# Kernel tuning notes

Measured on AMD Instinct MI355X. Metric: run time of the kernel, lower is better.

Reference implementation:

```python
import jax, jax.numpy as jnp
import numpy as np

N, L, HH, WW, E, NH = 8, 300, 96, 96, 256, 8


def setup_inputs() -> dict:
    key = jax.random.key(0)
    ks = jax.random.split(key, 9)
    return {
        "query_row": jax.random.normal(ks[0], (N, L, E), dtype=jnp.float32),
        "query_col": jax.random.normal(ks[1], (N, L, E), dtype=jnp.float32),
        "key_row": jax.random.normal(ks[2], (N, HH, WW, E), dtype=jnp.float32),
        "key_col": jax.random.normal(ks[3], (N, HH, WW, E), dtype=jnp.float32),
        "value": jax.random.normal(ks[4], (N, HH, WW, E), dtype=jnp.float32),
        "in_proj_weight": jax.random.normal(ks[5], (5 * E, E), dtype=jnp.float32) * 0.02,
        "in_proj_bias": jax.random.normal(ks[6], (5 * E,), dtype=jnp.float32) * 0.02,
        "out_proj_weight": jax.random.normal(ks[7], (E, E), dtype=jnp.float32) * 0.02,
        "out_proj_bias": jax.random.normal(ks[8], (E,), dtype=jnp.float32) * 0.02,
        "num_heads": NH,
    }


def reference(query_row, query_col, key_row, key_col, value,
              in_proj_weight, in_proj_bias, out_proj_weight, out_proj_bias,
              num_heads):
    bsz, tgt_len, embed_dim = query_row.shape
    head_dim = embed_dim // num_heads
    scaling = float(head_dim) ** -0.5

    def proj(x, i):
        w = in_proj_weight[i * embed_dim:(i + 1) * embed_dim]
        b = in_proj_bias[i * embed_dim:(i + 1) * embed_dim]
        return x @ w.T + b

    q_row = proj(query_row, 0) * scaling          # (N, L, E)
    q_col = proj(query_col, 1) * scaling          # (N, L, E)
    k_row = proj(key_row, 2).mean(axis=1)         # mean over H -> (N, W, E)
    k_col = proj(key_col, 3).mean(axis=2)         # mean over W -> (N, H, E)
    v = proj(value, 4)                            # (N, H, W, E)

    heads = lambda t: t.reshape(*t.shape[:-1], num_heads, head_dim)
    qr, qc, kr, kc = heads(q_row), heads(q_col), heads(k_row), heads(k_col)
    vh = heads(v)                                 # (N, H, W, nh, hd)

    # additive row/col decomposed scores -> independent softmaxes
    w_row = jax.nn.softmax(jnp.einsum('blnd,bwnd->bnlw', qr, kr), axis=-1)  # (N,nh,L,W)
    w_col = jax.nn.softmax(jnp.einsum('blnd,bhnd->bnlh', qc, kc), axis=-1)  # (N,nh,L,H)

    # contract col weights with value over H, then row weights over W
    tmp = jnp.einsum('bnlh,bhwnd->bnlwd', w_col, vh)       # (N,nh,L,W,hd)
    out = jnp.einsum('bnlw,bnlwd->blnd', w_row, tmp)       # (N,L,nh,hd)
    out = out.reshape(bsz, tgt_len, embed_dim).transpose(1, 0, 2)  # (L,N,E)
    return out @ out_proj_weight.T + out_proj_bias
```

## Files before the change

### kernel.cpp

```cpp
#include <hip/hip_runtime.h>
#include <cstdint>


typedef __attribute__((ext_vector_type(8))) short short8v;
typedef __attribute__((ext_vector_type(4))) short short4v;
typedef __attribute__((ext_vector_type(4))) float f32x4;

#define SCALE_Q 0.17677669529663687f

#define GLL16(gp, lp)                                                   \
  __builtin_amdgcn_global_load_lds(                                     \
      (const __attribute__((address_space(1))) void*)(gp),              \
      (__attribute__((address_space(3))) void*)(lp), 16, 0, 0)

__device__ __forceinline__ unsigned short f2bf(float x) {
  unsigned int u = __builtin_bit_cast(unsigned int, x);
  u += 0x7FFFu + ((u >> 16) & 1u);
  return (unsigned short)(u >> 16);
}

__device__ __forceinline__ short8v pack8(const float4& fa, const float4& fb) {
  short8v v;
  v[0] = (short)f2bf(fa.x); v[1] = (short)f2bf(fa.y);
  v[2] = (short)f2bf(fa.z); v[3] = (short)f2bf(fa.w);
  v[4] = (short)f2bf(fb.x); v[5] = (short)f2bf(fb.y);
  v[6] = (short)f2bf(fb.z); v[7] = (short)f2bf(fb.w);
  return v;
}

__device__ __forceinline__ short8v pack8v(const f32x4& fa, const f32x4& fb) {
  short8v v;
  v[0] = (short)f2bf(fa[0]); v[1] = (short)f2bf(fa[1]);
  v[2] = (short)f2bf(fa[2]); v[3] = (short)f2bf(fa[3]);
  v[4] = (short)f2bf(fb[0]); v[5] = (short)f2bf(fb[1]);
  v[6] = (short)f2bf(fb[2]); v[7] = (short)f2bf(fb[3]);
  return v;
}

__global__ __launch_bounds__(256) void cvt_w_kernel(const float* __restrict__ w_in,
                                                    const float* __restrict__ w_out,
                                                    short* __restrict__ Wb) {
  int idx = blockIdx.x * 256 + threadIdx.x;
  float v = (idx < 327680) ? w_in[idx] : w_out[idx - 327680];
  Wb[idx] = (short)f2bf(v);
}

__global__ __launch_bounds__(256) void mean_over_h_v3(const float* __restrict__ in,
                                                      float* __restrict__ out) {
  __shared__ float4 part[256];
  int bw = blockIdx.x;
  int b = bw / 96, w = bw - b * 96;
  int t = threadIdx.x, e4 = t & 63, hq = t >> 6;
  const float4* p = (const float4*)(in + ((size_t)b * 9216 + w) * 256) + e4 +
                    (size_t)hq * 24 * 6144;
  float4 s = {0.f, 0.f, 0.f, 0.f};
#pragma unroll
  for (int i = 0; i < 24; ++i) {
    float4 v = p[(size_t)i * 6144];
    s.x += v.x; s.y += v.y; s.z += v.z; s.w += v.w;
  }
  part[t] = s;
  __syncthreads();
  if (t < 64) {
    float4 a = part[t], c = part[t + 64], d = part[t + 128], e = part[t + 192];
    float4 o;
    o.x = (a.x + c.x + d.x + e.x) * (1.f / 96.f);
    o.y = (a.y + c.y + d.y + e.y) * (1.f / 96.f);
    o.z = (a.z + c.z + d.z + e.z) * (1.f / 96.f);
    o.w = (a.w + c.w + d.w + e.w) * (1.f / 96.f);
    ((float4*)out)[(size_t)bw * 64 + t] = o;
  }
}

__global__ __launch_bounds__(256) void mean_over_w_v3(const float* __restrict__ in,
                                                      float* __restrict__ out) {
  __shared__ float4 part[256];
  int bh = blockIdx.x;
  int t = threadIdx.x, e4 = t & 63, wq = t >> 6;
  const float4* p = (const float4*)(in + (size_t)bh * 24576) + e4 + (size_t)wq * 24 * 64;
  float4 s = {0.f, 0.f, 0.f, 0.f};
#pragma unroll
  for (int i = 0; i < 24; ++i) {
    float4 v = p[(size_t)i * 64];
    s.x += v.x; s.y += v.y; s.z += v.z; s.w += v.w;
  }
  part[t] = s;
  __syncthreads();
  if (t < 64) {
    float4 a = part[t], c = part[t + 64], d = part[t + 128], e = part[t + 192];
    float4 o;
    o.x = (a.x + c.x + d.x + e.x) * (1.f / 96.f);
    o.y = (a.y + c.y + d.y + e.y) * (1.f / 96.f);
    o.z = (a.z + c.z + d.z + e.z) * (1.f / 96.f);
    o.w = (a.w + c.w + d.w + e.w) * (1.f / 96.f);
    ((float4*)out)[(size_t)bh * 64 + t] = o;
  }
}

__global__ __launch_bounds__(256) void gemm_proj(
    const float* __restrict__ A0, const float* __restrict__ A1,
    const short* __restrict__ Wb, const float* __restrict__ bias,
    float* __restrict__ Cf, short* __restrict__ Cb0, short* __restrict__ Cb1,
    float scale, int mode) {
  __shared__ short As[32 * 264];
  int y = blockIdx.y;
  const float* A = y ? A1 : A0;
  short* Cb = y ? Cb1 : Cb0;
  const short* Wp = Wb + y * 65536;
  const float* bp = bias + y * 256;
  int t = threadIdx.x;
  int m0 = blockIdx.x * 32;
  int wave = t >> 6, lane = t & 63, r = lane & 15, g = lane >> 4;

  {
    int row = t >> 3, c0 = (t & 7) * 32;
    const float* ap = A + ((size_t)m0 + row) * 256 + c0;
    float4 ld[8];
#pragma unroll
    for (int j = 0; j < 8; ++j) ld[j] = *(const float4*)(ap + j * 4);
    short* dst = &As[row * 264 + c0];
#pragma unroll
    for (int j = 0; j < 4; ++j)
      *(short8v*)(dst + j * 8) = pack8(ld[2 * j], ld[2 * j + 1]);
  }
  __syncthreads();

  f32x4 acc[2][4] = {};
  const short* wbase = Wp + (size_t)(wave * 64 + r) * 256;
#pragma unroll
  for (int ks = 0; ks < 8; ++ks) {
    short8v af0 = *(const short8v*)&As[r * 264 + ks * 32 + g * 8];
    short8v af1 = *(const short8v*)&As[(16 + r) * 264 + ks * 32 + g * 8];
    short8v bf[4];
#pragma unroll
    for (int nf = 0; nf < 4; ++nf)
      bf[nf] = *(const short8v*)(wbase + nf * 16 * 256 + ks * 32 + g * 8);
#pragma unroll
    for (int nf = 0; nf < 4; ++nf) {
      acc[0][nf] = __builtin_amdgcn_mfma_f32_16x16x32_bf16(af0, bf[nf], acc[0][nf], 0, 0, 0);
      acc[1][nf] = __builtin_amdgcn_mfma_f32_16x16x32_bf16(af1, bf[nf], acc[1][nf], 0, 0, 0);
    }
  }

#pragma unroll
  for (int mf = 0; mf < 2; ++mf)
#pragma unroll
    for (int nf = 0; nf < 4; ++nf) {
      int nn = wave * 64 + nf * 16 + r;
      float bval = bp[nn];
#pragma unroll
      for (int i = 0; i < 4; ++i) {
        int m = m0 + mf * 16 + g * 4 + i;
        float val = (acc[mf][nf][i] + bval) * scale;
        if (mode == 1) {
          int bb = m / 300, ll = m - bb * 300;
          Cf[((size_t)ll * 8 + bb) * 256 + nn] = val;
        } else {
          Cb[(size_t)m * 256 + nn] = (short)f2bf(val);
        }
      }
    }
}

__global__ __launch_bounds__(256, 2) void vproj_kernel(
    const float* __restrict__ A, const short* __restrict__ Wb,
    const float* __restrict__ bias, short* __restrict__ vvT) {
  __shared__ float Asf[2][16][256];
  __shared__ short Ts[256 * 36];
  int t = threadIdx.x;
  int wave = t >> 6, lane = t & 63, r = lane & 15, g = lane >> 4;
  int tile0 = blockIdx.x * 8;

  short8v bf[8][4];
  const short* wbase = Wb + (size_t)(wave * 64 + r) * 256;
#pragma unroll
  for (int ks = 0; ks < 8; ++ks)
#pragma unroll
    for (int nf = 0; nf < 4; ++nf)
      bf[ks][nf] = *(const short8v*)(wbase + nf * 16 * 256 + ks * 32 + g * 8);

  float bias_v[4];
#pragma unroll
  for (int nf = 0; nf < 4; ++nf) bias_v[nf] = bias[wave * 64 + nf * 16 + r];

  {
    const float* gsrc = A + (size_t)tile0 * 16 * 256;
#pragma unroll
    for (int i = 0; i < 4; ++i) {
      int row = wave * 4 + i;
      const float* gp = gsrc + row * 256 + ((lane ^ (row & 7)) << 2);
      GLL16(gp, &Asf[0][row][0]);
    }
  }
  __syncthreads();

  for (int tt = 0; tt < 8; ++tt) {
    int cur = tt & 1;
    if (tt < 7) {
      const float* gsrc = A + (size_t)(tile0 + tt + 1) * 16 * 256;
#pragma unroll
      for (int i = 0; i < 4; ++i) {
        int row = wave * 4 + i;
        const float* gp = gsrc + row * 256 + ((lane ^ (row & 7)) << 2);
        GLL16(gp, &Asf[cur ^ 1][row][0]);
      }
    }

    f32x4 acc[4] = {};
    const float* base = &Asf[cur][r][0];
    int sw = r & 7;
#pragma unroll
    for (int ks = 0; ks < 8; ++ks) {
      int gr = ks * 8 + g * 2;
      f32x4 lo = *(const f32x4*)(base + ((gr ^ sw) << 2));
      f32x4 hi = *(const f32x4*)(base + (((gr + 1) ^ sw) << 2));
      short8v af = pack8v(lo, hi);
#pragma unroll
      for (int nf = 0; nf < 4; ++nf)
        acc[nf] = __builtin_amdgcn_mfma_f32_16x16x32_bf16(af, bf[ks][nf], acc[nf], 0, 0, 0);
    }

#pragma unroll
    for (int nf = 0; nf < 4; ++nf) {
      int nn = wave * 64 + nf * 16 + r;
      float bv = bias_v[nf];
      short4v o;
      o[0] = (short)f2bf(acc[nf][0] + bv);
      o[1] = (short)f2bf(acc[nf][1] + bv);
      o[2] = (short)f2bf(acc[nf][2] + bv);
      o[3] = (short)f2bf(acc[nf][3] + bv);
      *(short4v*)&Ts[nn * 36 + cur * 16 + g * 4] = o;
    }
    asm volatile("" ::: "memory");
    if (tt & 1) {
      int m0 = (tile0 + tt - 1) * 16;
      int b_ = m0 / 9216, hw0 = m0 - b_ * 9216;
      short* gdst = vvT + (size_t)(b_ * 8 + (t >> 5)) * 294912 +
                    (size_t)(t & 31) * 9216 + hw0;
#pragma unroll
      for (int j = 0; j < 4; ++j) {
        short4v lo = *(const short4v*)&Ts[t * 36 + j * 8];
        short4v hi = *(const short4v*)&Ts[t * 36 + j * 8 + 4];
        short8v v;
        v[0] = lo[0]; v[1] = lo[1]; v[2] = lo[2]; v[3] = lo[3];
        v[4] = hi[0]; v[5] = hi[1]; v[6] = hi[2]; v[7] = hi[3];
        *(short8v*)(gdst + j * 8) = v;
      }
      asm volatile("" ::: "memory");
    }
    __syncthreads();
  }
}

__global__ __launch_bounds__(64) void scores_softmax_v2(
    const short* __restrict__ qrb, const short* __restrict__ qcb,
    const short* __restrict__ krb, const short* __restrict__ kcb,
    short* __restrict__ wrowB, float* __restrict__ wcolT) {
  int lchunk = blockIdx.x, bn = blockIdx.y, kind = blockIdx.z;
  int b = bn >> 3, n = bn & 7;
  int lane = threadIdx.x;
  int r = lane & 15, g = lane >> 4;
  const short* qb = kind ? qcb : qrb;
  const short* kb = kind ? kcb : krb;
  int l0 = lchunk * 80;

  short8v a[5], bfr[6];
#pragma unroll
  for (int lf = 0; lf < 5; ++lf) {
    int l = l0 + lf * 16 + r;
    if (l > 299) l = 299;
    a[lf] = *(const short8v*)(qb + ((size_t)b * 300 + l) * 256 + n * 32 + g * 8);
  }
#pragma unroll
  for (int f = 0; f < 6; ++f)
    bfr[f] = *(const short8v*)(kb + ((size_t)b * 96 + f * 16 + r) * 256 + n * 32 + g * 8);

  f32x4 c[5][6];
#pragma unroll
  for (int lf = 0; lf < 5; ++lf)
#pragma unroll
    for (int f = 0; f < 6; ++f) {
      f32x4 z = {};
      c[lf][f] = __builtin_amdgcn_mfma_f32_16x16x32_bf16(a[lf], bfr[f], z, 0, 0, 0);
    }

#pragma unroll
  for (int lf = 0; lf < 5; ++lf)
#pragma unroll
    for (int i = 0; i < 4; ++i) {
      float m = c[lf][0][i];
#pragma unroll
      for (int f = 1; f < 6; ++f) m = fmaxf(m, c[lf][f][i]);
#pragma unroll
      for (int mask = 1; mask <= 8; mask <<= 1) m = fmaxf(m, __shfl_xor(m, mask, 64));
      float e[6], s = 0.f;
#pragma unroll
      for (int f = 0; f < 6; ++f) { e[f] = __expf(c[lf][f][i] - m); s += e[f]; }
#pragma unroll
      for (int mask = 1; mask <= 8; mask <<= 1) s += __shfl_xor(s, mask, 64);
      float inv = 1.f / s;
#pragma unroll
      for (int f = 0; f < 6; ++f) c[lf][f][i] = e[f] * inv;
    }

  if (kind == 0) {
#pragma unroll
    for (int lf = 0; lf < 5; ++lf)
#pragma unroll
      for (int i = 0; i < 4; ++i) {
        int l = l0 + lf * 16 + g * 4 + i;
        bool ok = (l < 300);
#pragma unroll
        for (int f = 0; f < 6; ++f) {
          float wv = ok ? c[lf][f][i] : 0.f;
          wrowB[((size_t)bn * 320 + l) * 96 + f * 16 + r] = (short)f2bf(wv);
        }
      }
  } else {
#pragma unroll
    for (int lf = 0; lf < 5; ++lf)
#pragma unroll
      for (int f = 0; f < 6; ++f) {
        int l = l0 + lf * 16 + g * 4;
        f32x4 wv = c[lf][f];
#pragma unroll
        for (int i = 0; i < 4; ++i) if (l + i >= 300) wv[i] = 0.f;
        *(f32x4*)(wcolT + ((size_t)bn * 96 + f * 16 + r) * 320 + l) = wv;
      }
  }
}

__global__ __launch_bounds__(512) void attn_kernel(
    const short* __restrict__ wrowB, const float* __restrict__ wcolT,
    const short* __restrict__ vvT, float* __restrict__ ao) {
  __shared__ f32x4 cmb[3][2][4][64];
  int lh = blockIdx.x, n = blockIdx.y, b = blockIdx.z;
  int bn = b * 8 + n;
  int t = threadIdx.x, wave = t >> 6, lane = t & 63;
  int df = wave & 1, hh = wave >> 1;
  int lbase = lh * 64;
  int r = lane & 15, g = lane >> 4;

  short8v a[4][3];
  const short* wr = wrowB + (size_t)bn * 320 * 96;
#pragma unroll
  for (int lf = 0; lf < 4; ++lf)
#pragma unroll
    for (int ks = 0; ks < 3; ++ks)
      a[lf][ks] = *(const short8v*)(wr + (lbase + lf * 16 + r) * 96 + ks * 32 + g * 8);

  const short* vb = vvT + (size_t)bn * 294912 + (size_t)(df * 16 + r) * 9216 + hh * 24 * 96;
  const float* wcb = wcolT + ((size_t)bn * 96 + hh * 24) * 320 + lbase + g * 4;

  f32x4 acc[4] = {};
  short8v b0[3], b1[3];
  f32x4 w0[4], w1[4];
#pragma unroll
  for (int ks = 0; ks < 3; ++ks) b0[ks] = *(const short8v*)(vb + ks * 32 + g * 8);
#pragma unroll
  for (int lf = 0; lf < 4; ++lf) w0[lf] = *(const f32x4*)(wcb + lf * 16);

  for (int h2 = 0; h2 < 12; ++h2) {
    int h = h2 * 2;
#pragma unroll
    for (int ks = 0; ks < 3; ++ks) b1[ks] = *(const short8v*)(vb + (h + 1) * 96 + ks * 32 + g * 8);
#pragma unroll
    for (int lf = 0; lf < 4; ++lf) w1[lf] = *(const f32x4*)(wcb + (h + 1) * 320 + lf * 16);
    {
      f32x4 R[4] = {};
#pragma unroll
      for (int ks = 0; ks < 3; ++ks)
#pragma unroll
        for (int lf = 0; lf < 4; ++lf)
          R[lf] = __builtin_amdgcn_mfma_f32_16x16x32_bf16(a[lf][ks], b0[ks], R[lf], 0, 0, 0);
#pragma unroll
      for (int lf = 0; lf < 4; ++lf) acc[lf] += w0[lf] * R[lf];
    }
    if (h2 < 11) {
#pragma unroll
      for (int ks = 0; ks < 3; ++ks) b0[ks] = *(const short8v*)(vb + (h + 2) * 96 + ks * 32 + g * 8);
#pragma unroll
      for (int lf = 0; lf < 4; ++lf) w0[lf] = *(const f32x4*)(wcb + (h + 2) * 320 + lf * 16);
    }
    {
      f32x4 R[4] = {};
#pragma unroll
      for (int ks = 0; ks < 3; ++ks)
#pragma unroll
        for (int lf = 0; lf < 4; ++lf)
          R[lf] = __builtin_amdgcn_mfma_f32_16x16x32_bf16(a[lf][ks], b1[ks], R[lf], 0, 0, 0);
#pragma unroll
      for (int lf = 0; lf < 4; ++lf) acc[lf] += w1[lf] * R[lf];
    }
  }

  if (hh > 0) {
#pragma unroll
    for (int lf = 0; lf < 4; ++lf) cmb[hh - 1][df][lf][lane] = acc[lf];
  }
  __syncthreads();
  if (hh == 0) {
#pragma unroll
    for (int lf = 0; lf < 4; ++lf) {
      f32x4 o = acc[lf];
#pragma unroll
      for (int q = 0; q < 3; ++q) o += cmb[q][df][lf][lane];
#pragma unroll
      for (int i = 0; i < 4; ++i) {
        int l = lbase + lf * 16 + g * 4 + i;
        if (l < 300)
          ao[((size_t)b * 300 + l) * 256 + n * 32 + df * 16 + r] = o[i];
      }
    }
  }
}

extern "C" void kernel_launch(void* const* d_in, const int* in_sizes, int n_in,
                              void* d_out, int out_size, void* d_ws, size_t ws_size,
                              hipStream_t stream) {
  const float* query_row = (const float*)d_in[0];
  const float* query_col = (const float*)d_in[1];
  const float* key_row   = (const float*)d_in[2];
  const float* key_col   = (const float*)d_in[3];
  const float* value     = (const float*)d_in[4];
  const float* W         = (const float*)d_in[5];
  const float* Bv        = (const float*)d_in[6];
  const float* Wout      = (const float*)d_in[7];
  const float* Bout      = (const float*)d_in[8];

  float* ws = (float*)d_ws;
  float* krm   = ws;
  float* kcm   = krm + 196608;
  float* ao    = kcm + 196608;
  float* wcolT = ao + 614400;
  short* qrb   = (short*)(wcolT + 1966080);
  short* qcb   = qrb + 614400;
  short* krb   = qcb + 614400;
  short* kcb   = krb + 196608;
  short* wrowB = kcb + 196608;
  short* vvT   = wrowB + 1966080;
  short* Wb    = vvT + 18874368;

  cvt_w_kernel<<<1536, 256, 0, stream>>>(W, Wout, Wb);
  mean_over_h_v3<<<768, 256, 0, stream>>>(key_row, krm);
  mean_over_w_v3<<<768, 256, 0, stream>>>(key_col, kcm);
  gemm_proj<<<dim3(75, 2), 256, 0, stream>>>(query_row, query_col, Wb, Bv,
                                             nullptr, qrb, qcb, SCALE_Q, 3);
  gemm_proj<<<dim3(24, 2), 256, 0, stream>>>(krm, kcm, Wb + 131072, Bv + 512,
                                             nullptr, krb, kcb, 1.f, 3);
  vproj_kernel<<<576, 256, 0, stream>>>(value, Wb + 262144, Bv + 1024, vvT);
  scores_softmax_v2<<<dim3(4, 64, 2), 64, 0, stream>>>(qrb, qcb, krb, kcb, wrowB, wcolT);
  attn_kernel<<<dim3(5, 8, 8), 512, 0, stream>>>(wrowB, wcolT, vvT, ao);
  gemm_proj<<<dim3(75, 1), 256, 0, stream>>>(ao, nullptr, Wb + 327680, Bout,
                                             (float*)d_out, nullptr, nullptr, 1.f, 1);
}
```

Before: 171.0 us.

## Restructure value projection to split channels across blocks and load A directly

The value-projection kernel now splits the 256 output channels into two groups across blocks, so each wave holds half as many weight fragments. Activations are read straight from global memory into registers instead of through double-buffered LDS with global_load_lds. Each wave does its own transpose-to-store through a private LDS slice, which removes the block-wide barrier. Float-to-bf16 packing now uses the hardware v_cvt_pk_bf16_f32 instruction. The trade-off is that each activation row is read twice (once per channel group), and with no LDS staging the global loads are less coalesced.

```diff
diff --git a/kernel.cpp b/kernel.cpp
--- a/kernel.cpp
+++ b/kernel.cpp
@@ -7,16 +7,33 @@
 typedef __attribute__((ext_vector_type(4))) float f32x4;
 
 #define SCALE_Q 0.17677669529663687f
-
-#define GLL16(gp, lp)                                                   \
-  __builtin_amdgcn_global_load_lds(                                     \
-      (const __attribute__((address_space(1))) void*)(gp),              \
-      (__attribute__((address_space(3))) void*)(lp), 16, 0, 0)
 
 __device__ __forceinline__ unsigned short f2bf(float x) {
   unsigned int u = __builtin_bit_cast(unsigned int, x);
   u += 0x7FFFu + ((u >> 16) & 1u);
   return (unsigned short)(u >> 16);
+}
+
+__device__ __forceinline__ unsigned int cvtpk(float a, float b) {
+  unsigned int r;
+  asm("v_cvt_pk_bf16_f32 %0, %1, %2" : "=v"(r) : "v"(a), "v"(b));
+  return r;
+}
+
+__device__ __forceinline__ short8v pack8cvt(const f32x4& lo, const f32x4& hi) {
+  union { short8v s; unsigned int u[4]; } z;
+  z.u[0] = cvtpk(lo[0], lo[1]);
+  z.u[1] = cvtpk(lo[2], lo[3]);
+  z.u[2] = cvtpk(hi[0], hi[1]);
+  z.u[3] = cvtpk(hi[2], hi[3]);
+  return z.s;
+}
+
+__device__ __forceinline__ short4v pack4cvt(float a, float b, float c, float d) {
+  union { short4v s; unsigned int u[2]; } z;
+  z.u[0] = cvtpk(a, b);
+  z.u[1] = cvtpk(c, d);
+  return z.s;
 }
 
 __device__ __forceinline__ short8v pack8(const float4& fa, const float4& fb) {
@@ -25,15 +42,6 @@
   v[2] = (short)f2bf(fa.z); v[3] = (short)f2bf(fa.w);
   v[4] = (short)f2bf(fb.x); v[5] = (short)f2bf(fb.y);
   v[6] = (short)f2bf(fb.z); v[7] = (short)f2bf(fb.w);
-  return v;
-}
-
-__device__ __forceinline__ short8v pack8v(const f32x4& fa, const f32x4& fb) {
-  short8v v;
-  v[0] = (short)f2bf(fa[0]); v[1] = (short)f2bf(fa[1]);
-  v[2] = (short)f2bf(fa[2]); v[3] = (short)f2bf(fa[3]);
-  v[4] = (short)f2bf(fb[0]); v[5] = (short)f2bf(fb[1]);
-  v[6] = (short)f2bf(fb[2]); v[7] = (short)f2bf(fb[3]);
   return v;
 }
 
@@ -162,93 +170,65 @@
     }
 }
 
-__global__ __launch_bounds__(256, 2) void vproj_kernel(
+__global__ __launch_bounds__(256) void vproj_kernel(
     const float* __restrict__ A, const short* __restrict__ Wb,
     const float* __restrict__ bias, short* __restrict__ vvT) {
-  __shared__ float Asf[2][16][256];
-  __shared__ short Ts[256 * 36];
+  __shared__ short Ts[4 * 32 * 36];
   int t = threadIdx.x;
   int wave = t >> 6, lane = t & 63, r = lane & 15, g = lane >> 4;
-  int tile0 = blockIdx.x * 8;
-
-  short8v bf[8][4];
-  const short* wbase = Wb + (size_t)(wave * 64 + r) * 256;
+  int chgrp = blockIdx.x & 1, tg = blockIdx.x >> 1;
+  int chbase = chgrp * 128 + wave * 32;
+
+  short8v bf[8][2];
 #pragma unroll
   for (int ks = 0; ks < 8; ++ks)
 #pragma unroll
-    for (int nf = 0; nf < 4; ++nf)
-      bf[ks][nf] = *(const short8v*)(wbase + nf * 16 * 256 + ks * 32 + g * 8);
-
-  float bias_v[4];
-#pragma unroll
-  for (int nf = 0; nf < 4; ++nf) bias_v[nf] = bias[wave * 64 + nf * 16 + r];
-
-  {
-    const float* gsrc = A + (size_t)tile0 * 16 * 256;
-#pragma unroll
-    for (int i = 0; i < 4; ++i) {
-      int row = wave * 4 + i;
-      const float* gp = gsrc + row * 256 + ((lane ^ (row & 7)) << 2);
-      GLL16(gp, &Asf[0][row][0]);
-    }
-  }
-  __syncthreads();
-
-  for (int tt = 0; tt < 8; ++tt) {
-    int cur = tt & 1;
-    if (tt < 7) {
-      const float* gsrc = A + (size_t)(tile0 + tt + 1) * 16 * 256;
-#pragma unroll
-      for (int i = 0; i < 4; ++i) {
-        int row = wave * 4 + i;
-        const float* gp = gsrc + row * 256 + ((lane ^ (row & 7)) << 2);
-        GLL16(gp, &Asf[cur ^ 1][row][0]);
-      }
-    }
-
-    f32x4 acc[4] = {};
-    const float* base = &Asf[cur][r][0];
-    int sw = r & 7;
+    for (int nf = 0; nf < 2; ++nf)
+      bf[ks][nf] = *(const short8v*)(Wb + (size_t)(chbase + nf * 16 + r) * 256 +
+                                     ks * 32 + g * 8);
+  float bias_v[2];
+#pragma unroll
+  for (int nf = 0; nf < 2; ++nf) bias_v[nf] = bias[chbase + nf * 16 + r];
+
+  short* tsw = &Ts[wave * 1152];
+  int chg = chbase + (lane & 31);
+  int half = lane >> 5;
+  const short* tsr = tsw + (lane & 31) * 36 + half * 16;
+  short* vbase = vvT + (size_t)(chg >> 5) * 294912 + (size_t)(chg & 31) * 9216 +
+                 half * 16;
+
+  for (int tt = 0; tt < 18; ++tt) {
+    int m0 = (tg * 18 + tt) * 16;
+    const float* ap = A + (size_t)(m0 + r) * 256 + g * 8;
+    float4 ld[16];
 #pragma unroll
     for (int ks = 0; ks < 8; ++ks) {
-      int gr = ks * 8 + g * 2;
-      f32x4 lo = *(const f32x4*)(base + ((gr ^ sw) << 2));
-      f32x4 hi = *(const f32x4*)(base + (((gr + 1) ^ sw) << 2));
-      short8v af = pack8v(lo, hi);
-#pragma unroll
-      for (int nf = 0; nf < 4; ++nf)
-        acc[nf] = __builtin_amdgcn_mfma_f32_16x16x32_bf16(af, bf[ks][nf], acc[nf], 0, 0, 0);
-    }
-
-#pragma unroll
-    for (int nf = 0; nf < 4; ++nf) {
-      int nn = wave * 64 + nf * 16 + r;
+      ld[2 * ks]     = *(const float4*)(ap + ks * 32);
+      ld[2 * ks + 1] = *(const float4*)(ap + ks * 32 + 4);
+    }
+    f32x4 acc[2] = {};
+#pragma unroll
+    for (int ks = 0; ks < 8; ++ks) {
+      short8v af = pack8cvt(*(const f32x4*)&ld[2 * ks], *(const f32x4*)&ld[2 * ks + 1]);
+      acc[0] = __builtin_amdgcn_mfma_f32_16x16x32_bf16(af, bf[ks][0], acc[0], 0, 0, 0);
+      acc[1] = __builtin_amdgcn_mfma_f32_16x16x32_bf16(af, bf[ks][1], acc[1], 0, 0, 0);
+    }
+    int par = tt & 1;
+#pragma unroll
+    for (int nf = 0; nf < 2; ++nf) {
       float bv = bias_v[nf];
-      short4v o;
-      o[0] = (short)f2bf(acc[nf][0] + bv);
-      o[1] = (short)f2bf(acc[nf][1] + bv);
-      o[2] = (short)f2bf(acc[nf][2] + bv);
-      o[3] = (short)f2bf(acc[nf][3] + bv);
-      *(short4v*)&Ts[nn * 36 + cur * 16 + g * 4] = o;
+      *(short4v*)&tsw[(nf * 16 + r) * 36 + par * 16 + g * 4] =
+          pack4cvt(acc[nf][0] + bv, acc[nf][1] + bv, acc[nf][2] + bv, acc[nf][3] + bv);
     }
     asm volatile("" ::: "memory");
-    if (tt & 1) {
-      int m0 = (tile0 + tt - 1) * 16;
-      int b_ = m0 / 9216, hw0 = m0 - b_ * 9216;
-      short* gdst = vvT + (size_t)(b_ * 8 + (t >> 5)) * 294912 +
-                    (size_t)(t & 31) * 9216 + hw0;
-#pragma unroll
-      for (int j = 0; j < 4; ++j) {
-        short4v lo = *(const short4v*)&Ts[t * 36 + j * 8];
-        short4v hi = *(const short4v*)&Ts[t * 36 + j * 8 + 4];
-        short8v v;
-        v[0] = lo[0]; v[1] = lo[1]; v[2] = lo[2]; v[3] = lo[3];
-        v[4] = hi[0]; v[5] = hi[1]; v[6] = hi[2]; v[7] = hi[3];
-        *(short8v*)(gdst + j * 8) = v;
-      }
+    if (par) {
+      int m0e = m0 - 16;
+      int b_ = m0e / 9216, hw0 = m0e - b_ * 9216;
+      short* gdst = vbase + (size_t)b_ * 8 * 294912 + hw0;
+      *(short8v*)(gdst)     = *(const short8v*)(tsr);
+      *(short8v*)(gdst + 8) = *(const short8v*)(tsr + 8);
       asm volatile("" ::: "memory");
     }
-    __syncthreads();
   }
 }
 
@@ -448,7 +428,7 @@
                                              nullptr, qrb, qcb, SCALE_Q, 3);
   gemm_proj<<<dim3(24, 2), 256, 0, stream>>>(krm, kcm, Wb + 131072, Bv + 512,
                                              nullptr, krb, kcb, 1.f, 3);
-  vproj_kernel<<<576, 256, 0, stream>>>(value, Wb + 262144, Bv + 1024, vvT);
+  vproj_kernel<<<512, 256, 0, stream>>>(value, Wb + 262144, Bv + 1024, vvT);
   scores_softmax_v2<<<dim3(4, 64, 2), 64, 0, stream>>>(qrb, qcb, krb, kcb, wrowB, wcolT);
   attn_kernel<<<dim3(5, 8, 8), 512, 0, stream>>>(wrowB, wcolT, vvT, ao);
   gemm_proj<<<dim3(75, 1), 256, 0, stream>>>(ao, nullptr, Wb + 327680, Bout,
```

Result: slower. 197.1 us (+15.3%).
